# Kernel optimization log

Measured on AMD Instinct MI355X. Metric: run time of the kernel, lower is better.

The kernel has to match this reference:

```python
import jax, jax.numpy as jnp
import numpy as np

HIDDEN = 2048
NUM_HEADS = 32
NUM_KV_HEADS = 8
HEAD_DIM = HIDDEN // NUM_HEADS  # 64
GROUP = NUM_HEADS // NUM_KV_HEADS  # 4
B, S = 2, 2048


def setup_inputs() -> dict:
    key = jax.random.key(0)
    ks = jax.random.split(key, 9)
    sc = 0.02
    kv_dim = NUM_KV_HEADS * HEAD_DIM
    return {
        "x": jax.random.normal(ks[0], (B, S, HIDDEN), jnp.float32),
        # weights stored as [in, out] (transpose of torch Linear.weight)
        "Wq": jax.random.normal(ks[1], (HIDDEN, HIDDEN), jnp.float32) * sc,
        "bq": jnp.zeros((HIDDEN,), jnp.float32),
        "Wk": jax.random.normal(ks[2], (HIDDEN, kv_dim), jnp.float32) * sc,
        "bk": jnp.zeros((kv_dim,), jnp.float32),
        "Wv": jax.random.normal(ks[3], (HIDDEN, kv_dim), jnp.float32) * sc,
        "bv": jnp.zeros((kv_dim,), jnp.float32),
        "Wo": jax.random.normal(ks[4], (HIDDEN, HIDDEN), jnp.float32) * sc,
        "bo": jnp.zeros((HIDDEN,), jnp.float32),
    }


def reference(x, Wq, bq, Wk, bk, Wv, bv, Wo, bo):
    b, s, _ = x.shape
    q = (x @ Wq + bq).reshape(b, s, NUM_KV_HEADS, GROUP, HEAD_DIM)
    k = (x @ Wk + bk).reshape(b, s, NUM_KV_HEADS, HEAD_DIM)
    v = (x @ Wv + bv).reshape(b, s, NUM_KV_HEADS, HEAD_DIM)
    scale = 1.0 / jnp.sqrt(jnp.asarray(HEAD_DIM, x.dtype))
    # scores: [b, g(kv heads), r(q per group), s(query), t(key)]
    scores = jnp.einsum("bsgrd,btgd->bgrst", q, k) * scale
    attn = jax.nn.softmax(scores, axis=-1)  # dropout rate 0 -> identity
    out = jnp.einsum("bgrst,btgd->bsgrd", attn, v).reshape(b, s, HIDDEN)
    return out @ Wo + bo
```

## Files before the change

kernel.cpp:

```cpp
#include <hip/hip_runtime.h>

#define HIDDEN 2048
#define NHEADS 32
#define NKV 8
#define HD 64
#define BATCH 2
#define SEQ 2048
#define KVD 512
#define BSZ 4096
#define QKVD 3072

typedef __bf16 bfx8 __attribute__((ext_vector_type(8)));
typedef __bf16 bfx4 __attribute__((ext_vector_type(4)));
typedef float f32x4 __attribute__((ext_vector_type(4)));
typedef short sx4v __attribute__((ext_vector_type(4)));

#define QSCALE 0.1803368801111204f

#if defined(__AMDGCN__) && __has_builtin(__builtin_amdgcn_mfma_f32_16x16x16_bf16)
#define MFMA16(a, b, c) __builtin_amdgcn_mfma_f32_16x16x16_bf16(a, b, c, 0, 0, 0)
#else
#define MFMA16(a, b, c)                                                    \
    __builtin_amdgcn_mfma_f32_16x16x16bf16_1k(__builtin_bit_cast(sx4v, (a)), \
                                              __builtin_bit_cast(sx4v, (b)), (c), 0, 0, 0)
#endif

__device__ __forceinline__ void gl_lds16(const __bf16* g, __bf16* l) {
    __builtin_amdgcn_global_load_lds(
        (const __attribute__((address_space(1))) unsigned int*)g,
        (__attribute__((address_space(3))) unsigned int*)l, 16, 0, 0);
}

__global__ __launch_bounds__(256) void cvt_bf16(const float* __restrict__ src,
                                                __bf16* __restrict__ dst, int n4) {
    int i = blockIdx.x * 256 + threadIdx.x;
    if (i >= n4) return;
    float4 f = ((const float4*)src)[i];
    bfx4 o = {(__bf16)f.x, (__bf16)f.y, (__bf16)f.z, (__bf16)f.w};
    *(bfx4*)(dst + (size_t)i * 4) = o;
}

__device__ __forceinline__ void tcvt_tile(const float* __restrict__ src,
                                          __bf16* __restrict__ dst,
                                          int R, int C, int tx, int ty,
                                          float (*tile)[65], int t, float mul) {
    int br = ty * 64, bc = tx * 64;
    {
        int r = t >> 4, c = (t & 15) * 4;
#pragma unroll
        for (int i = 0; i < 4; ++i) {
            float4 v = *(const float4*)(&src[(long)(br + r + i * 16) * C + bc + c]);
            tile[r + i * 16][c + 0] = v.x * mul;
            tile[r + i * 16][c + 1] = v.y * mul;
            tile[r + i * 16][c + 2] = v.z * mul;
            tile[r + i * 16][c + 3] = v.w * mul;
        }
    }
    __syncthreads();
    {
        int d = t >> 2, tt0 = (t & 3) * 16;
        bfx8 o0, o1;
#pragma unroll
        for (int j = 0; j < 8; ++j) o0[j] = (__bf16)tile[tt0 + j][d];
#pragma unroll
        for (int j = 0; j < 8; ++j) o1[j] = (__bf16)tile[tt0 + 8 + j][d];
        *(bfx8*)(&dst[(long)(bc + d) * R + br + tt0]) = o0;
        *(bfx8*)(&dst[(long)(bc + d) * R + br + tt0 + 8]) = o1;
    }
}

__global__ __launch_bounds__(256) void prep(const float* __restrict__ Wq,
                                            const float* __restrict__ Wk,
                                            const float* __restrict__ Wv,
                                            const float* __restrict__ Wo,
                                            const float* __restrict__ bq,
                                            const float* __restrict__ bk,
                                            const float* __restrict__ bv,
                                            __bf16* __restrict__ wqkvt,
                                            __bf16* __restrict__ wot,
                                            float* __restrict__ bqkv) {
    __shared__ float tile[64][65];
    int idx = blockIdx.x, t = threadIdx.x;
    if (idx < 1024) {
        tcvt_tile(Wq, wqkvt, HIDDEN, HIDDEN, idx & 31, idx >> 5, tile, t, QSCALE);
    } else if (idx < 1280) {
        int l = idx - 1024;
        tcvt_tile(Wk, wqkvt + (size_t)HIDDEN * HIDDEN, HIDDEN, KVD, l & 7, l >> 3, tile, t, 1.0f);
    } else if (idx < 1536) {
        int l = idx - 1280;
        tcvt_tile(Wv, wqkvt + (size_t)(HIDDEN + KVD) * HIDDEN, HIDDEN, KVD, l & 7, l >> 3, tile, t, 1.0f);
    } else if (idx < 2560) {
        int l = idx - 1536;
        tcvt_tile(Wo, wot, HIDDEN, HIDDEN, l & 31, l >> 5, tile, t, 1.0f);
    } else {
        int i = (idx - 2560) * 256 + t;
        if (i < QKVD) {
            float v = (i < HIDDEN) ? bq[i] * QSCALE
                                   : (i < HIDDEN + KVD ? bk[i - HIDDEN] : bv[i - HIDDEN - KVD]);
            bqkv[i] = v;
        }
    }
}

__global__ __launch_bounds__(256) void transpose_v(const __bf16* __restrict__ qkv,
                                                   __bf16* __restrict__ vt) {
    __shared__ __bf16 tile[64][65];
    int t = threadIdx.x;
    int nb0 = blockIdx.x * 64;
    int bh = blockIdx.y;
    int b = bh >> 3, kv = bh & 7;
    {
        int tt = t >> 2, c0 = (t & 3) * 16;
        const __bf16* p = &qkv[(long)(b * SEQ + nb0 + tt) * QKVD + HIDDEN + KVD + kv * HD + c0];
        bfx8 a0 = *(const bfx8*)(p);
        bfx8 a1 = *(const bfx8*)(p + 8);
#pragma unroll
        for (int j = 0; j < 8; ++j) tile[tt][c0 + j] = a0[j];
#pragma unroll
        for (int j = 0; j < 8; ++j) tile[tt][c0 + 8 + j] = a1[j];
    }
    __syncthreads();
    {
        int d = t >> 2, tt0 = (t & 3) * 16;
        bfx8 o0, o1;
#pragma unroll
        for (int j = 0; j < 8; ++j) o0[j] = tile[tt0 + j][d];
#pragma unroll
        for (int j = 0; j < 8; ++j) o1[j] = tile[tt0 + 8 + j][d];
        __bf16* q = &vt[((long)bh * HD + d) * SEQ + nb0 + tt0];
        *(bfx8*)(q) = o0;
        *(bfx8*)(q + 8) = o1;
    }
}

template <bool OUT_BF16>
__global__ __launch_bounds__(256, 3) void gemm128(const __bf16* __restrict__ A,
                                                  const __bf16* __restrict__ Bt,
                                                  const float* __restrict__ bias,
                                                  void* __restrict__ C,
                                                  int M, int N, int K) {
    __shared__ __align__(16) __bf16 As[2][128 * 32];
    __shared__ __align__(16) __bf16 Bs[2][128 * 32];
    int t = threadIdx.x;
    int w = t >> 6, lane = t & 63;
    int lrow = lane & 15, quad = lane >> 4;
    long m0 = (long)blockIdx.y * 128, n0 = (long)blockIdx.x * 128;
    int wr = (w >> 1) * 64, wc = (w & 1) * 64;
    f32x4 acc[4][4] = {};
    int srow = t >> 2, scol = (((t & 3) ^ ((t >> 3) & 3))) * 8;
    int sA = (lrow >> 1) & 3;
    const __bf16* Ag = A + (m0 + srow) * (long)K + scol;
    const __bf16* Bg = Bt + (n0 + srow) * (long)K + scol;
#define STAGE_G(kb, buf)                                                      \
    {                                                                         \
        _Pragma("unroll") for (int c = 0; c < 2; ++c) {                       \
            gl_lds16(Ag + (long)c * 64 * K + (kb), &As[buf][c * 2048 + w * 512]); \
            gl_lds16(Bg + (long)c * 64 * K + (kb), &Bs[buf][c * 2048 + w * 512]); \
        }                                                                     \
    }
    STAGE_G(0, 0);
    int nk = K >> 5;
    for (int it = 0; it < nk; ++it) {
        __syncthreads();
        if (it + 1 < nk) STAGE_G((it + 1) * 32, (it + 1) & 1);
        const __bf16* Ab = &As[it & 1][0];
        const __bf16* Bb = &Bs[it & 1][0];
        bfx8 af[4], bfr[4];
#pragma unroll
        for (int i = 0; i < 4; ++i)
            af[i] = *(const bfx8*)&Ab[(wr + i * 16 + lrow) * 32 + ((quad ^ sA) * 8)];
#pragma unroll
        for (int j = 0; j < 4; ++j)
            bfr[j] = *(const bfx8*)&Bb[(wc + j * 16 + lrow) * 32 + ((quad ^ sA) * 8)];
#pragma unroll
        for (int i = 0; i < 4; ++i)
#pragma unroll
            for (int j = 0; j < 4; ++j)
                acc[i][j] = __builtin_amdgcn_mfma_f32_16x16x32_bf16(af[i], bfr[j], acc[i][j], 0, 0, 0);
    }
#undef STAGE_G
#pragma unroll
    for (int j = 0; j < 4; ++j) {
        long col = n0 + wc + j * 16 + lrow;
        float bv = bias[col];
#pragma unroll
        for (int i = 0; i < 4; ++i) {
#pragma unroll
            for (int r = 0; r < 4; ++r) {
                long row = m0 + wr + i * 16 + quad * 4 + r;
                float val = acc[i][j][r] + bv;
                if (OUT_BF16)
                    ((__bf16*)C)[row * N + col] = (__bf16)val;
                else
                    ((float*)C)[row * N + col] = val;
            }
        }
    }
}

__global__ __launch_bounds__(256, 4) void attn(const __bf16* __restrict__ QKV,
                                               const __bf16* __restrict__ Vt,
                                               __bf16* __restrict__ O) {
    __shared__ __align__(16) __bf16 Ks[2][64 * 64];
    __shared__ __align__(16) __bf16 Vs[2][64 * 64];
    int t = threadIdx.x;
    int w = t >> 6, lane = t & 63;
    int lrow = lane & 15, quad = lane >> 4;
    int qb = blockIdx.x, bh = blockIdx.y;
    int b = bh >> 5, h = bh & 31, kv = h >> 2;
    int q0 = qb * 128 + w * 32;

    bfx8 qf[2][2];
#pragma unroll
    for (int i = 0; i < 2; ++i)
#pragma unroll
        for (int kk = 0; kk < 2; ++kk)
            qf[i][kk] = *(const bfx8*)(QKV + (long)(b * SEQ + q0 + i * 16 + lrow) * QKVD +
                                       h * HD + kk * 32 + quad * 8);

    int srow = t >> 2, scol = (((t & 3) ^ ((t >> 3) & 3))) * 8;
    int sA = (lrow >> 1) & 3;
    const __bf16* kg = QKV + (long)(b * SEQ + srow) * QKVD + HIDDEN + kv * HD + scol;
    const __bf16* vg = Vt + ((long)(b * NKV + kv) * HD + srow) * SEQ + scol;
#define STAGE_KV(nb, buf)                                                          \
    {                                                                              \
        _Pragma("unroll") for (int c = 0; c < 2; ++c) {                            \
            gl_lds16(kg + (long)(nb)*QKVD + c * 32, &Ks[buf][c * 2048 + w * 512]); \
            gl_lds16(vg + (nb) + c * 32, &Vs[buf][c * 2048 + w * 512]);            \
        }                                                                          \
    }
    STAGE_KV(0, 0);

    f32x4 accO[4][2] = {};
    float lacc[2] = {0.f, 0.f};

    for (int it = 0; it < SEQ / 64; ++it) {
        __syncthreads();
        if (it + 1 < SEQ / 64) STAGE_KV((it + 1) * 64, (it + 1) & 1);
        const __bf16* Kb = &Ks[it & 1][0];
        const __bf16* Vb = &Vs[it & 1][0];
#pragma unroll
        for (int tt = 0; tt < 4; ++tt) {
            bfx8 ka0 = *(const bfx8*)&Kb[tt * 512 + lrow * 32 + ((quad ^ sA) * 8)];
            bfx8 ka1 = *(const bfx8*)&Kb[2048 + tt * 512 + lrow * 32 + ((quad ^ sA) * 8)];
            f32x4 s2[2];
#pragma unroll
            for (int i = 0; i < 2; ++i) {
                f32x4 z = {};
                z = __builtin_amdgcn_mfma_f32_16x16x32_bf16(ka0, qf[i][0], z, 0, 0, 0);
                s2[i] = __builtin_amdgcn_mfma_f32_16x16x32_bf16(ka1, qf[i][1], z, 0, 0, 0);
            }
            bfx4 pb[2];
#pragma unroll
            for (int i = 0; i < 2; ++i) {
                float p0 = __builtin_amdgcn_exp2f(s2[i][0]);
                float p1 = __builtin_amdgcn_exp2f(s2[i][1]);
                float p2 = __builtin_amdgcn_exp2f(s2[i][2]);
                float p3 = __builtin_amdgcn_exp2f(s2[i][3]);
                lacc[i] += (p0 + p1) + (p2 + p3);
                bfx4 pp = {(__bf16)p0, (__bf16)p1, (__bf16)p2, (__bf16)p3};
                pb[i] = pp;
            }
            int vbase = (tt >> 1) * 2048 + lrow * 32 +
                        ((((tt & 1) * 2 + (quad >> 1)) ^ sA) * 8) + (quad & 1) * 4;
#pragma unroll
            for (int dt = 0; dt < 4; ++dt) {
                bfx4 va = *(const bfx4*)&Vb[vbase + dt * 512];
#pragma unroll
                for (int i = 0; i < 2; ++i)
                    accO[dt][i] = MFMA16(va, pb[i], accO[dt][i]);
            }
        }
    }
    float inv[2];
#pragma unroll
    for (int i = 0; i < 2; ++i) {
        float l = lacc[i];
        l += __shfl_xor(l, 16);
        l += __shfl_xor(l, 32);
        inv[i] = 1.0f / l;
    }
#pragma unroll
    for (int i = 0; i < 2; ++i) {
        long row = (long)(b * SEQ + q0 + i * 16 + lrow);
#pragma unroll
        for (int dt = 0; dt < 4; ++dt) {
            bfx4 o4 = {(__bf16)(accO[dt][i][0] * inv[i]), (__bf16)(accO[dt][i][1] * inv[i]),
                       (__bf16)(accO[dt][i][2] * inv[i]), (__bf16)(accO[dt][i][3] * inv[i])};
            *(bfx4*)&O[row * HIDDEN + h * HD + dt * 16 + quad * 4] = o4;
        }
    }
#undef STAGE_KV
}

extern "C" void kernel_launch(void* const* d_in, const int* in_sizes, int n_in,
                              void* d_out, int out_size, void* d_ws, size_t ws_size,
                              hipStream_t stream) {
    const float* x  = (const float*)d_in[0];
    const float* Wq = (const float*)d_in[1];
    const float* bq = (const float*)d_in[2];
    const float* Wk = (const float*)d_in[3];
    const float* bk = (const float*)d_in[4];
    const float* Wv = (const float*)d_in[5];
    const float* bv = (const float*)d_in[6];
    const float* Wo = (const float*)d_in[7];
    const float* bo = (const float*)d_in[8];
    float* out = (float*)d_out;

    __bf16* ws    = (__bf16*)d_ws;
    __bf16* xb    = ws;
    __bf16* wqkvt = xb + (size_t)BSZ * HIDDEN;
    __bf16* wot   = wqkvt + (size_t)QKVD * HIDDEN;
    __bf16* qkv   = wot + (size_t)HIDDEN * HIDDEN;
    __bf16* vt_   = qkv + (size_t)BSZ * QKVD;
    __bf16* ab_   = vt_ + (size_t)BSZ * KVD;
    float*  bqkv  = (float*)(ab_ + (size_t)BSZ * HIDDEN);

    cvt_bf16<<<(BSZ * HIDDEN / 4 + 255) / 256, 256, 0, stream>>>(x, xb, BSZ * HIDDEN / 4);
    prep<<<2560 + (QKVD + 255) / 256, 256, 0, stream>>>(Wq, Wk, Wv, Wo, bq, bk, bv,
                                                        wqkvt, wot, bqkv);

    gemm128<true><<<dim3(QKVD / 128, BSZ / 128), 256, 0, stream>>>(xb, wqkvt, bqkv, qkv, BSZ, QKVD, HIDDEN);

    transpose_v<<<dim3(SEQ / 64, BATCH * NKV), 256, 0, stream>>>(qkv, vt_);
    attn<<<dim3(SEQ / 128, BATCH * NHEADS), 256, 0, stream>>>(qkv, vt_, ab_);

    gemm128<false><<<dim3(HIDDEN / 128, BSZ / 128), 256, 0, stream>>>(ab_, wot, bo, out, BSZ, HIDDEN, HIDDEN);
}
```

Measured before the change: 328.9 us.

## Use 16x16x32 MFMA for PV product via permlane-swapped P fragments

Processes two 16-key score tiles per step and rearranges the packed bf16 probabilities across lanes with v_permlane32/16_swap. This lets the P·V product use the K=32 MFMA instead of two K=16 MFMAs, with 16-byte V reads from LDS. The aim is to halve the number of PV MFMA issues and LDS read instructions. The cost is extra permlane instructions and higher register pressure from keeping two score tiles live. Correctness depends on the lane permutation matching the V layout in LDS.

```diff
diff --git a/kernel.cpp b/kernel.cpp
--- a/kernel.cpp
+++ b/kernel.cpp
@@ -12,23 +12,21 @@
 
 typedef __bf16 bfx8 __attribute__((ext_vector_type(8)));
 typedef __bf16 bfx4 __attribute__((ext_vector_type(4)));
+typedef __bf16 bfx2 __attribute__((ext_vector_type(2)));
 typedef float f32x4 __attribute__((ext_vector_type(4)));
-typedef short sx4v __attribute__((ext_vector_type(4)));
+typedef unsigned int ux4 __attribute__((ext_vector_type(4)));
 
 #define QSCALE 0.1803368801111204f
-
-#if defined(__AMDGCN__) && __has_builtin(__builtin_amdgcn_mfma_f32_16x16x16_bf16)
-#define MFMA16(a, b, c) __builtin_amdgcn_mfma_f32_16x16x16_bf16(a, b, c, 0, 0, 0)
-#else
-#define MFMA16(a, b, c)                                                    \
-    __builtin_amdgcn_mfma_f32_16x16x16bf16_1k(__builtin_bit_cast(sx4v, (a)), \
-                                              __builtin_bit_cast(sx4v, (b)), (c), 0, 0, 0)
-#endif
 
 __device__ __forceinline__ void gl_lds16(const __bf16* g, __bf16* l) {
     __builtin_amdgcn_global_load_lds(
         (const __attribute__((address_space(1))) unsigned int*)g,
         (__attribute__((address_space(3))) unsigned int*)l, 16, 0, 0);
+}
+
+__device__ __forceinline__ unsigned int pk2(float lo, float hi) {
+    bfx2 v = {(__bf16)lo, (__bf16)hi};
+    return __builtin_bit_cast(unsigned int, v);
 }
 
 __global__ __launch_bounds__(256) void cvt_bf16(const float* __restrict__ src,
@@ -240,35 +238,47 @@
         const __bf16* Kb = &Ks[it & 1][0];
         const __bf16* Vb = &Vs[it & 1][0];
 #pragma unroll
-        for (int tt = 0; tt < 4; ++tt) {
-            bfx8 ka0 = *(const bfx8*)&Kb[tt * 512 + lrow * 32 + ((quad ^ sA) * 8)];
-            bfx8 ka1 = *(const bfx8*)&Kb[2048 + tt * 512 + lrow * 32 + ((quad ^ sA) * 8)];
-            f32x4 s2[2];
+        for (int ch = 0; ch < 2; ++ch) {
+            f32x4 s2[2][2];
+#pragma unroll
+            for (int tp = 0; tp < 2; ++tp) {
+                int tt = ch * 2 + tp;
+                bfx8 ka0 = *(const bfx8*)&Kb[tt * 512 + lrow * 32 + ((quad ^ sA) * 8)];
+                bfx8 ka1 = *(const bfx8*)&Kb[2048 + tt * 512 + lrow * 32 + ((quad ^ sA) * 8)];
+#pragma unroll
+                for (int i = 0; i < 2; ++i) {
+                    f32x4 z = {};
+                    z = __builtin_amdgcn_mfma_f32_16x16x32_bf16(ka0, qf[i][0], z, 0, 0, 0);
+                    s2[tp][i] = __builtin_amdgcn_mfma_f32_16x16x32_bf16(ka1, qf[i][1], z, 0, 0, 0);
+                }
+            }
+            bfx8 p8v[2];
 #pragma unroll
             for (int i = 0; i < 2; ++i) {
-                f32x4 z = {};
-                z = __builtin_amdgcn_mfma_f32_16x16x32_bf16(ka0, qf[i][0], z, 0, 0, 0);
-                s2[i] = __builtin_amdgcn_mfma_f32_16x16x32_bf16(ka1, qf[i][1], z, 0, 0, 0);
+                float pa0 = __builtin_amdgcn_exp2f(s2[0][i][0]);
+                float pa1 = __builtin_amdgcn_exp2f(s2[0][i][1]);
+                float pa2 = __builtin_amdgcn_exp2f(s2[0][i][2]);
+                float pa3 = __builtin_amdgcn_exp2f(s2[0][i][3]);
+                float pb0 = __builtin_amdgcn_exp2f(s2[1][i][0]);
+                float pb1 = __builtin_amdgcn_exp2f(s2[1][i][1]);
+                float pb2 = __builtin_amdgcn_exp2f(s2[1][i][2]);
+                float pb3 = __builtin_amdgcn_exp2f(s2[1][i][3]);
+                lacc[i] += ((pa0 + pa1) + (pa2 + pa3)) + ((pb0 + pb1) + (pb2 + pb3));
+                unsigned int A0 = pk2(pa0, pa1), A1 = pk2(pa2, pa3);
+                unsigned int B0 = pk2(pb0, pb1), B1 = pk2(pb2, pb3);
+                asm("v_permlane32_swap_b32 %0, %1" : "+v"(A0), "+v"(B0));
+                asm("v_permlane16_swap_b32 %0, %1" : "+v"(A0), "+v"(B0));
+                asm("v_permlane32_swap_b32 %0, %1" : "+v"(A1), "+v"(B1));
+                asm("v_permlane16_swap_b32 %0, %1" : "+v"(A1), "+v"(B1));
+                ux4 pw = {A0, A1, B0, B1};
+                p8v[i] = __builtin_bit_cast(bfx8, pw);
             }
-            bfx4 pb[2];
-#pragma unroll
-            for (int i = 0; i < 2; ++i) {
-                float p0 = __builtin_amdgcn_exp2f(s2[i][0]);
-                float p1 = __builtin_amdgcn_exp2f(s2[i][1]);
-                float p2 = __builtin_amdgcn_exp2f(s2[i][2]);
-                float p3 = __builtin_amdgcn_exp2f(s2[i][3]);
-                lacc[i] += (p0 + p1) + (p2 + p3);
-                bfx4 pp = {(__bf16)p0, (__bf16)p1, (__bf16)p2, (__bf16)p3};
-                pb[i] = pp;
-            }
-            int vbase = (tt >> 1) * 2048 + lrow * 32 +
-                        ((((tt & 1) * 2 + (quad >> 1)) ^ sA) * 8) + (quad & 1) * 4;
 #pragma unroll
             for (int dt = 0; dt < 4; ++dt) {
-                bfx4 va = *(const bfx4*)&Vb[vbase + dt * 512];
+                bfx8 va = *(const bfx8*)&Vb[ch * 2048 + (dt * 16 + lrow) * 32 + ((quad ^ sA) * 8)];
 #pragma unroll
                 for (int i = 0; i < 2; ++i)
-                    accO[dt][i] = MFMA16(va, pb[i], accO[dt][i]);
+                    accO[dt][i] = __builtin_amdgcn_mfma_f32_16x16x32_bf16(va, p8v[i], accO[dt][i], 0, 0, 0);
             }
         }
     }
```

Result: faster. 313.0 us (-4.8%).
